# Kernel optimization log

Hardware: AMD Instinct MI355X
Metric: run time of the kernel (lower is better)

Reference implementation:

```python
import jax, jax.numpy as jnp
import numpy as np

C = 64          # num_channels
DEPTH = 9       # dilation_depth
REPEAT = 2      # dilation_repeat
K = 2           # kernel_size
DILATIONS = [2 ** j for _ in range(REPEAT) for j in range(DEPTH)]
L = len(DILATIONS)  # 18 gated layers


def causal_conv(x, w, b, dilation):
    # x: [B, Cin, T], w: [Cout, Cin, K] -> [B, Cout, T] with causal (left) padding
    pad = (w.shape[-1] - 1) * dilation
    y = jax.lax.conv_general_dilated(
        x, w, window_strides=(1,), padding=[(pad, 0)],
        rhs_dilation=(dilation,), dimension_numbers=("NCH", "OIH", "NCH"))
    return y + b[None, :, None]


def setup_inputs() -> dict:
    key = jax.random.key(0)
    ks = jax.random.split(key, 9)
    s = 0.1
    x = jax.random.normal(ks[0], (4, 1, 65536), dtype=jnp.float32)
    in_w = jax.random.normal(ks[1], (C, 1, 1), dtype=jnp.float32) * s
    in_b = jax.random.normal(ks[2], (C,), dtype=jnp.float32) * s
    hid_w = jax.random.normal(ks[3], (L, 2 * C, C, K), dtype=jnp.float32) * s
    hid_b = jax.random.normal(ks[4], (L, 2 * C), dtype=jnp.float32) * s
    res_w = jax.random.normal(ks[5], (L, C, C, 1), dtype=jnp.float32) * s
    res_b = jax.random.normal(ks[6], (L, C), dtype=jnp.float32) * s
    mix_w = jax.random.normal(ks[7], (1, C * L, 1), dtype=jnp.float32) * s
    mix_b = jax.random.normal(ks[8], (1,), dtype=jnp.float32) * s
    return {"x": x, "in_w": in_w, "in_b": in_b, "hid_w": hid_w, "hid_b": hid_b,
            "res_w": res_w, "res_b": res_b, "mix_w": mix_w, "mix_b": mix_b}


def reference(x, in_w, in_b, hid_w, hid_b, res_w, res_b, mix_w, mix_b):
    # Input 1x1 conv: [B,1,T] -> [B,C,T]
    out = causal_conv(x, in_w, in_b, 1)
    skips = []
    for i, d in enumerate(DILATIONS):
        xi = out
        h = causal_conv(xi, hid_w[i], hid_b[i], d)       # [B, 2C, T]
        gated = jnp.tanh(h[:, :C]) * jax.nn.sigmoid(h[:, C:])  # [B, C, T]
        skips.append(gated)
        out = causal_conv(gated, res_w[i], res_b[i], 1) + xi    # residual
    skip = jnp.concatenate(skips, axis=1)                # [B, C*L, T]
    return causal_conv(skip, mix_w, mix_b, 1)            # [B, 1, T]
```

## Files before the change

### kernel.cpp

```cpp
#include <hip/hip_runtime.h>
#include <hip/hip_bf16.h>
#include <math.h>

#define NCH 64
#define T_LEN 65536
#define NLAYER 18

typedef __attribute__((ext_vector_type(8))) short bf16x8;
typedef __attribute__((ext_vector_type(4))) short bf16x4;
typedef __attribute__((ext_vector_type(4))) float f32x4;

static __device__ __forceinline__ float bf2f(short s) {
    union { short u[2]; float f; } v;
    v.u[0] = 0; v.u[1] = s;
    return v.f;
}
static __device__ __forceinline__ short f2bf(float f) {
    __hip_bfloat16 h = __float2bfloat16(f);
    return *(short*)&h;
}

__global__ void convert_weights_kernel(const float* __restrict__ hid_w,
                                       const float* __restrict__ res_w,
                                       __hip_bfloat16* __restrict__ whid,
                                       __hip_bfloat16* __restrict__ wres) {
    int gid = blockIdx.x * 256 + threadIdx.x;
    if (gid < NLAYER * 128 * 128) {
        int l   = gid >> 14;
        int rem = gid & 16383;
        int o   = rem >> 7;
        int k   = rem & 127;
        float v = (k < 64)
            ? hid_w[((l * 128 + o) * 64 + k) * 2]
            : hid_w[((l * 128 + o) * 64 + (k - 64)) * 2 + 1];
        whid[gid] = __float2bfloat16(v);
    }
    if (gid < NLAYER * 64 * 64) {
        wres[gid] = __float2bfloat16(res_w[gid]);
    }
}

__global__ __launch_bounds__(256, 2) void fused6_kernel(
    const void* __restrict__ src,
    __hip_bfloat16* __restrict__ next,
    float* __restrict__ acc,
    const __hip_bfloat16* __restrict__ whid_all,
    const float* __restrict__ hb_all,
    const __hip_bfloat16* __restrict__ wres_all,
    const float* __restrict__ rb_all,
    const float* __restrict__ mix_w,
    const float* __restrict__ in_w,
    const float* __restrict__ in_b,
    int lbase, int is_first) {
    __shared__ __align__(16) __hip_bfloat16 A[192 * 72];
    __shared__ __align__(16) __hip_bfloat16 G[192 * 72];

    const int b    = blockIdx.x >> 9;
    const int widx = blockIdx.x & 511;
    const int t0   = widx << 7;
    const int tw   = t0 - 64;

    const int tid  = threadIdx.x;
    const int lane = tid & 63;
    const int w4   = tid >> 6;
    const int l15  = lane & 15;
    const int quad = lane >> 4;
    const int m0   = w4 * 16;
    const int rr   = tid >> 3;
    const int co   = (tid & 7) * 8;

    if (is_first) {
        const float* x = (const float*)src;
        float iw[8], ib[8];
#pragma unroll
        for (int j = 0; j < 8; ++j) { iw[j] = in_w[co + j]; ib[j] = in_b[co + j]; }
#pragma unroll
        for (int round = 0; round < 6; ++round) {
            int r  = round * 32 + rr;
            int gt = tw + r;
            bf16x8 v = {0, 0, 0, 0, 0, 0, 0, 0};
            if (gt >= 0) {
                float xv = x[(size_t)b * T_LEN + gt];
#pragma unroll
                for (int j = 0; j < 8; ++j) v[j] = f2bf(iw[j] * xv + ib[j]);
            }
            *(bf16x8*)(&A[r * 72 + co]) = v;
        }
    } else {
        const __hip_bfloat16* prev = (const __hip_bfloat16*)src;
#pragma unroll
        for (int round = 0; round < 6; ++round) {
            int r  = round * 32 + rr;
            int gt = tw + r;
            bf16x8 v = {0, 0, 0, 0, 0, 0, 0, 0};
            if (gt >= 0)
                v = *(const bf16x8*)(prev + ((size_t)b * T_LEN + gt) * NCH + co);
            *(bf16x8*)(&A[r * 72 + co]) = v;
        }
    }

    float skacc0 = 0.f, skacc1 = 0.f;

#pragma unroll 1
    for (int l = 0; l < 6; ++l) {
        const int d = 1 << l;
        const __hip_bfloat16* whid = whid_all + (size_t)(lbase + l) * 16384;
        const __hip_bfloat16* wres = wres_all + (size_t)(lbase + l) * 4096;
        const float* hb = hb_all + (lbase + l) * 128;
        const float* rb = rb_all + (lbase + l) * 64;
        const float* mw = mix_w + (lbase + l) * 64;

        bf16x8 aT[4], aS[4], aR[2];
        {
            const __hip_bfloat16* whT = whid + (size_t)(m0 + l15) * 128 + quad * 8;
            const __hip_bfloat16* whS = whT + 64 * 128;
#pragma unroll
            for (int k = 0; k < 4; ++k) {
                aT[k] = *(const bf16x8*)(whT + k * 32);
                aS[k] = *(const bf16x8*)(whS + k * 32);
            }
            const __hip_bfloat16* wrA = wres + (size_t)(m0 + l15) * 64 + quad * 8;
            aR[0] = *(const bf16x8*)(wrA);
            aR[1] = *(const bf16x8*)(wrA + 32);
        }
        f32x4 biasT, biasS, biasR;
#pragma unroll
        for (int r = 0; r < 4; ++r) {
            biasT[r] = hb[m0 + quad * 4 + r];
            biasS[r] = hb[64 + m0 + quad * 4 + r];
            biasR[r] = rb[m0 + quad * 4 + r];
        }
        float mwq[16];
#pragma unroll
        for (int k = 0; k < 4; ++k) {
            float4 m4 = *(const float4*)(mw + quad * 16 + k * 4);
            mwq[k * 4 + 0] = m4.x; mwq[k * 4 + 1] = m4.y;
            mwq[k * 4 + 2] = m4.z; mwq[k * 4 + 3] = m4.w;
        }

        __syncthreads();

#pragma unroll
        for (int ct = 0; ct < 3; ++ct) {
            f32x4 accT[4], accS[4];
#pragma unroll
            for (int nt = 0; nt < 4; ++nt) { accT[nt] = biasT; accS[nt] = biasS; }
#pragma unroll
            for (int ks = 0; ks < 4; ++ks) {
                const int koff = (ks & 1) * 32 + quad * 8;
#pragma unroll
                for (int nt = 0; nt < 4; ++nt) {
                    int trow = ct * 64 + nt * 16 + l15;
                    int prow = trow - d;  prow = prow < 0 ? 0 : prow;
                    int row  = (ks < 2) ? prow : trow;
                    bf16x8 bx = *(const bf16x8*)(&A[row * 72 + koff]);
                    accT[nt] = __builtin_amdgcn_mfma_f32_16x16x32_bf16(aT[ks], bx, accT[nt], 0, 0, 0);
                    accS[nt] = __builtin_amdgcn_mfma_f32_16x16x32_bf16(aS[ks], bx, accS[nt], 0, 0, 0);
                }
            }
#pragma unroll
            for (int nt = 0; nt < 4; ++nt) {
                int trow = ct * 64 + nt * 16 + l15;
                bf16x4 gv;
#pragma unroll
                for (int r = 0; r < 4; ++r) {
                    float e2 = __expf(2.f * accT[nt][r]);
                    float th = 1.f - 2.f * __builtin_amdgcn_rcpf(e2 + 1.f);
                    float sg = __builtin_amdgcn_rcpf(1.f + __expf(-accS[nt][r]));
                    gv[r] = f2bf(th * sg);
                }
                *(bf16x4*)(&G[trow * 72 + m0 + quad * 4]) = gv;
            }
        }
        __syncthreads();

#pragma unroll
        for (int ct = 0; ct < 3; ++ct) {
            f32x4 accR[4];
#pragma unroll
            for (int nt = 0; nt < 4; ++nt) accR[nt] = biasR;
#pragma unroll
            for (int ks = 0; ks < 2; ++ks) {
                const int koff = ks * 32 + quad * 8;
#pragma unroll
                for (int nt = 0; nt < 4; ++nt) {
                    int trow = ct * 64 + nt * 16 + l15;
                    bf16x8 bx = *(const bf16x8*)(&G[trow * 72 + koff]);
                    accR[nt] = __builtin_amdgcn_mfma_f32_16x16x32_bf16(aR[ks], bx, accR[nt], 0, 0, 0);
                }
            }
#pragma unroll
            for (int nt = 0; nt < 4; ++nt) {
                int trow = ct * 64 + nt * 16 + l15;
                bf16x4 old = *(const bf16x4*)(&A[trow * 72 + m0 + quad * 4]);
                bool ok = (tw + trow) >= 0;
                bf16x4 ov;
#pragma unroll
                for (int r = 0; r < 4; ++r) {
                    float v = accR[nt][r] + bf2f(old[r]);
                    ov[r] = f2bf(ok ? v : 0.f);
                }
                *(bf16x4*)(&A[trow * 72 + m0 + quad * 4]) = ov;
            }
        }

#pragma unroll
        for (int s = 0; s < 2; ++s) {
            int p = 64 + w4 * 32 + s * 16 + l15;
            bf16x8 g0 = *(const bf16x8*)(&G[p * 72 + quad * 16]);
            bf16x8 g1 = *(const bf16x8*)(&G[p * 72 + quad * 16 + 8]);
            float sv = 0.f;
#pragma unroll
            for (int j = 0; j < 8; ++j) {
                sv += mwq[j]     * bf2f(g0[j]);
                sv += mwq[8 + j] * bf2f(g1[j]);
            }
            if (s == 0) skacc0 += sv; else skacc1 += sv;
        }
    }
    __syncthreads();

#pragma unroll
    for (int round = 0; round < 4; ++round) {
        int pr = round * 32 + rr;
        *(bf16x8*)(next + ((size_t)b * T_LEN + t0 + pr) * NCH + co) =
            *(const bf16x8*)(&A[(pr + 64) * 72 + co]);
    }

    skacc0 += __shfl_xor(skacc0, 16, 64);
    skacc0 += __shfl_xor(skacc0, 32, 64);
    skacc1 += __shfl_xor(skacc1, 16, 64);
    skacc1 += __shfl_xor(skacc1, 32, 64);
    if (quad == 0) {
        acc[(size_t)b * T_LEN + t0 + w4 * 32 + l15]      += skacc0;
        acc[(size_t)b * T_LEN + t0 + w4 * 32 + 16 + l15] += skacc1;
    }
}

__global__ __launch_bounds__(256, 2) void layer_mfma_kernel(
    const __hip_bfloat16* __restrict__ prev,
    __hip_bfloat16* __restrict__ next,
    float* __restrict__ acc,
    const __hip_bfloat16* __restrict__ whid,
    const float* __restrict__ hb,
    const __hip_bfloat16* __restrict__ wres,
    const float* __restrict__ rb,
    const float* __restrict__ mw,
    int d) {
    __shared__ __align__(16) __hip_bfloat16 Xp[64 * 72];
    __shared__ __align__(16) __hip_bfloat16 Xc[64 * 72];
    __shared__ __align__(16) __hip_bfloat16 Gt[64 * 72];

    const int t0   = blockIdx.x << 6;
    const int tid  = threadIdx.x;
    const int lane = tid & 63;
    const int w4   = tid >> 6;
    const int l15  = lane & 15;
    const int quad = lane >> 4;
    const int m0   = w4 * 16;
    const int rr = tid >> 3;
    const int co = (tid & 7) * 8;

    bf16x8 aT[4], aS[4], aR[2];
    {
        const __hip_bfloat16* whT = whid + (size_t)(m0 + l15) * 128 + quad * 8;
        const __hip_bfloat16* whS = whT + 64 * 128;
#pragma unroll
        for (int k = 0; k < 4; ++k) {
            aT[k] = *(const bf16x8*)(whT + k * 32);
            aS[k] = *(const bf16x8*)(whS + k * 32);
        }
        const __hip_bfloat16* wrA = wres + (size_t)(m0 + l15) * 64 + quad * 8;
        aR[0] = *(const bf16x8*)(wrA);
        aR[1] = *(const bf16x8*)(wrA + 32);
    }
    f32x4 biasT, biasS, biasR;
#pragma unroll
    for (int r = 0; r < 4; ++r) {
        biasT[r] = hb[m0 + quad * 4 + r];
        biasS[r] = hb[64 + m0 + quad * 4 + r];
        biasR[r] = rb[m0 + quad * 4 + r];
    }
    float mwq[16];
#pragma unroll
    for (int j = 0; j < 16; ++j) mwq[j] = mw[quad * 16 + j];

    bf16x8 pc[2], pp[2];
#define LOAD_TILE(b)                                                          \
    do {                                                                      \
        const __hip_bfloat16* pb = prev + ((size_t)(b) * T_LEN + t0) * NCH;   \
        _Pragma("unroll")                                                     \
        for (int pass = 0; pass < 2; ++pass) {                                \
            int r = pass * 32 + rr;                                           \
            pc[pass] = *(const bf16x8*)(pb + r * NCH + co);                   \
            int tp = t0 + r - d;                                              \
            bf16x8 z = {0, 0, 0, 0, 0, 0, 0, 0};                              \
            pp[pass] = z;                                                     \
            if (tp >= 0)                                                      \
                pp[pass] = *(const bf16x8*)(prev +                            \
                    ((size_t)(b) * T_LEN + tp) * NCH + co);                   \
        }                                                                     \
    } while (0)

    LOAD_TILE(0);

#pragma unroll
    for (int b = 0; b < 4; ++b) {
#pragma unroll
        for (int pass = 0; pass < 2; ++pass) {
            int r = pass * 32 + rr;
            *(bf16x8*)(&Xc[r * 72 + co]) = pc[pass];
            *(bf16x8*)(&Xp[r * 72 + co]) = pp[pass];
        }
        __syncthreads();

        if (b < 3) LOAD_TILE(b + 1);

        f32x4 accT[4], accS[4];
#pragma unroll
        for (int nt = 0; nt < 4; ++nt) { accT[nt] = biasT; accS[nt] = biasS; }
#pragma unroll
        for (int ks = 0; ks < 4; ++ks) {
            const __hip_bfloat16* srcb = (ks < 2) ? Xp : Xc;
            const int kk = (ks & 1) * 32 + quad * 8;
#pragma unroll
            for (int nt = 0; nt < 4; ++nt) {
                bf16x8 bx = *(const bf16x8*)(&srcb[(nt * 16 + l15) * 72 + kk]);
                accT[nt] = __builtin_amdgcn_mfma_f32_16x16x32_bf16(aT[ks], bx, accT[nt], 0, 0, 0);
                accS[nt] = __builtin_amdgcn_mfma_f32_16x16x32_bf16(aS[ks], bx, accS[nt], 0, 0, 0);
            }
        }

#pragma unroll
        for (int nt = 0; nt < 4; ++nt) {
            int t = nt * 16 + l15;
#pragma unroll
            for (int r = 0; r < 4; ++r) {
                float e2 = __expf(2.f * accT[nt][r]);
                float th = 1.f - 2.f * __builtin_amdgcn_rcpf(e2 + 1.f);
                float sg = __builtin_amdgcn_rcpf(1.f + __expf(-accS[nt][r]));
                Gt[t * 72 + m0 + quad * 4 + r] = __float2bfloat16(th * sg);
            }
        }

        bf16x4 curres[4];
#pragma unroll
        for (int nt = 0; nt < 4; ++nt) {
            curres[nt] = *(const bf16x4*)(&Xc[(nt * 16 + l15) * 72 + m0 + quad * 4]);
        }
        __syncthreads();

        f32x4 accR[4];
#pragma unroll
        for (int nt = 0; nt < 4; ++nt) accR[nt] = biasR;
#pragma unroll
        for (int ks = 0; ks < 2; ++ks) {
            const int kk = ks * 32 + quad * 8;
#pragma unroll
            for (int nt = 0; nt < 4; ++nt) {
                bf16x8 bx = *(const bf16x8*)(&Gt[(nt * 16 + l15) * 72 + kk]);
                accR[nt] = __builtin_amdgcn_mfma_f32_16x16x32_bf16(aR[ks], bx, accR[nt], 0, 0, 0);
            }
        }

        __hip_bfloat16* nb = next + ((size_t)b * T_LEN + t0) * NCH;
#pragma unroll
        for (int nt = 0; nt < 4; ++nt) {
            int t = nt * 16 + l15;
            bf16x4 ov;
#pragma unroll
            for (int r = 0; r < 4; ++r) {
                ov[r] = f2bf(accR[nt][r] + bf2f(curres[nt][r]));
            }
            *(bf16x4*)(nb + t * NCH + m0 + quad * 4) = ov;
        }

        {
            int t = w4 * 16 + l15;
            bf16x8 g0 = *(const bf16x8*)(&Gt[t * 72 + quad * 16]);
            bf16x8 g1 = *(const bf16x8*)(&Gt[t * 72 + quad * 16 + 8]);
            float s = 0.f;
#pragma unroll
            for (int j = 0; j < 8; ++j) {
                s += mwq[j]     * bf2f(g0[j]);
                s += mwq[8 + j] * bf2f(g1[j]);
            }
            s += __shfl_xor(s, 16, 64);
            s += __shfl_xor(s, 32, 64);
            if (quad == 0)
                acc[(size_t)b * T_LEN + t0 + t] += s;
        }
    }
#undef LOAD_TILE
}

__global__ __launch_bounds__(256, 2) void last_layer_kernel(
    const __hip_bfloat16* __restrict__ prev,
    const float* __restrict__ acc,
    float* __restrict__ out,
    const __hip_bfloat16* __restrict__ whid,
    const float* __restrict__ hb,
    const float* __restrict__ mw,
    const float* __restrict__ mix_b,
    int d) {
    __shared__ __align__(16) __hip_bfloat16 Xp[64 * 72];
    __shared__ __align__(16) __hip_bfloat16 Xc[64 * 72];
    __shared__ float skb[4 * 64];

    const int t0   = blockIdx.x << 6;
    const int tid  = threadIdx.x;
    const int lane = tid & 63;
    const int w4   = tid >> 6;
    const int l15  = lane & 15;
    const int quad = lane >> 4;
    const int m0   = w4 * 16;
    const int rr = tid >> 3;
    const int co = (tid & 7) * 8;

    bf16x8 aT[4], aS[4];
    {
        const __hip_bfloat16* whT = whid + (size_t)(m0 + l15) * 128 + quad * 8;
        const __hip_bfloat16* whS = whT + 64 * 128;
#pragma unroll
        for (int k = 0; k < 4; ++k) {
            aT[k] = *(const bf16x8*)(whT + k * 32);
            aS[k] = *(const bf16x8*)(whS + k * 32);
        }
    }
    f32x4 biasT, biasS;
    float mwv[4];
#pragma unroll
    for (int r = 0; r < 4; ++r) {
        biasT[r] = hb[m0 + quad * 4 + r];
        biasS[r] = hb[64 + m0 + quad * 4 + r];
        mwv[r]   = mw[m0 + quad * 4 + r];
    }
    const float mb = mix_b[0];

    bf16x8 pc[2], pp[2];
#define LOAD_TILE(b)                                                          \
    do {                                                                      \
        const __hip_bfloat16* pb = prev + ((size_t)(b) * T_LEN + t0) * NCH;   \
        _Pragma("unroll")                                                     \
        for (int pass = 0; pass < 2; ++pass) {                                \
            int r = pass * 32 + rr;                                           \
            pc[pass] = *(const bf16x8*)(pb + r * NCH + co);                   \
            int tp = t0 + r - d;                                              \
            bf16x8 z = {0, 0, 0, 0, 0, 0, 0, 0};                              \
            pp[pass] = z;                                                     \
            if (tp >= 0)                                                      \
                pp[pass] = *(const bf16x8*)(prev +                            \
                    ((size_t)(b) * T_LEN + tp) * NCH + co);                   \
        }                                                                     \
    } while (0)

    LOAD_TILE(0);

#pragma unroll
    for (int b = 0; b < 4; ++b) {
#pragma unroll
        for (int pass = 0; pass < 2; ++pass) {
            int r = pass * 32 + rr;
            *(bf16x8*)(&Xc[r * 72 + co]) = pc[pass];
            *(bf16x8*)(&Xp[r * 72 + co]) = pp[pass];
        }
        __syncthreads();

        if (b < 3) LOAD_TILE(b + 1);

        f32x4 accT[4], accS[4];
#pragma unroll
        for (int nt = 0; nt < 4; ++nt) { accT[nt] = biasT; accS[nt] = biasS; }
#pragma unroll
        for (int ks = 0; ks < 4; ++ks) {
            const __hip_bfloat16* srcb = (ks < 2) ? Xp : Xc;
            const int kk = (ks & 1) * 32 + quad * 8;
#pragma unroll
            for (int nt = 0; nt < 4; ++nt) {
                bf16x8 bx = *(const bf16x8*)(&srcb[(nt * 16 + l15) * 72 + kk]);
                accT[nt] = __builtin_amdgcn_mfma_f32_16x16x32_bf16(aT[ks], bx, accT[nt], 0, 0, 0);
                accS[nt] = __builtin_amdgcn_mfma_f32_16x16x32_bf16(aS[ks], bx, accS[nt], 0, 0, 0);
            }
        }

#pragma unroll
        for (int nt = 0; nt < 4; ++nt) {
            float sv = 0.f;
#pragma unroll
            for (int r = 0; r < 4; ++r) {
                float e2 = __expf(2.f * accT[nt][r]);
                float th = 1.f - 2.f * __builtin_amdgcn_rcpf(e2 + 1.f);
                float sg = __builtin_amdgcn_rcpf(1.f + __expf(-accS[nt][r]));
                sv += mwv[r] * (th * sg);
            }
            sv += __shfl_xor(sv, 16, 64);
            sv += __shfl_xor(sv, 32, 64);
            if (quad == 0)
                skb[w4 * 64 + nt * 16 + l15] = sv;
        }
        __syncthreads();

        if (tid < 64) {
            float tot = skb[tid] + skb[64 + tid] + skb[128 + tid] + skb[192 + tid];
            out[(size_t)b * T_LEN + t0 + tid] =
                acc[(size_t)b * T_LEN + t0 + tid] + tot + mb;
        }
    }
#undef LOAD_TILE
}

extern "C" void kernel_launch(void* const* d_in, const int* in_sizes, int n_in,
                              void* d_out, int out_size, void* d_ws, size_t ws_size,
                              hipStream_t stream) {
    const float* x     = (const float*)d_in[0];
    const float* in_w  = (const float*)d_in[1];
    const float* in_b  = (const float*)d_in[2];
    const float* hid_w = (const float*)d_in[3];
    const float* hid_b = (const float*)d_in[4];
    const float* res_w = (const float*)d_in[5];
    const float* res_b = (const float*)d_in[6];
    const float* mix_w = (const float*)d_in[7];
    const float* mix_b = (const float*)d_in[8];
    float* out = (float*)d_out;

    const size_t act_elems = 4ull * T_LEN * NCH;
    __hip_bfloat16* actA = (__hip_bfloat16*)d_ws;
    __hip_bfloat16* actB = actA + act_elems;
    float* acc = (float*)(actB + act_elems);
    __hip_bfloat16* whid = (__hip_bfloat16*)(acc + 4ull * T_LEN);
    __hip_bfloat16* wres = whid + (size_t)NLAYER * 128 * 128;

    hipMemsetAsync(acc, 0, 4ull * T_LEN * sizeof(float), stream);

    convert_weights_kernel<<<1152, 256, 0, stream>>>(hid_w, res_w, whid, wres);

    fused6_kernel<<<2048, 256, 0, stream>>>(
        x, actA, acc, whid, hid_b, wres, res_b, mix_w, in_w, in_b, 0, 1);

    layer_mfma_kernel<<<1024, 256, 0, stream>>>(
        actA, actB, acc, whid + 6 * 16384, hid_b + 6 * 128,
        wres + 6 * 4096, res_b + 6 * 64, mix_w + 6 * 64, 64);
    layer_mfma_kernel<<<1024, 256, 0, stream>>>(
        actB, actA, acc, whid + 7 * 16384, hid_b + 7 * 128,
        wres + 7 * 4096, res_b + 7 * 64, mix_w + 7 * 64, 128);
    layer_mfma_kernel<<<1024, 256, 0, stream>>>(
        actA, actB, acc, whid + 8 * 16384, hid_b + 8 * 128,
        wres + 8 * 4096, res_b + 8 * 64, mix_w + 8 * 64, 256);

    fused6_kernel<<<2048, 256, 0, stream>>>(
        actB, actA, acc, whid, hid_b, wres, res_b, mix_w, in_w, in_b, 9, 0);

    layer_mfma_kernel<<<1024, 256, 0, stream>>>(
        actA, actB, acc, whid + 15 * 16384, hid_b + 15 * 128,
        wres + 15 * 4096, res_b + 15 * 64, mix_w + 15 * 64, 64);
    layer_mfma_kernel<<<1024, 256, 0, stream>>>(
        actB, actA, acc, whid + 16 * 16384, hid_b + 16 * 128,
        wres + 16 * 4096, res_b + 16 * 64, mix_w + 16 * 64, 128);

    last_layer_kernel<<<1024, 256, 0, stream>>>(
        actA, acc, out, whid + 17 * 16384, hid_b + 17 * 128,
        mix_w + 17 * 64, mix_b, 256);
}
```

Baseline: 559.0 us.

## Swizzle LDS tiles, fuse skip mix into gate epilogue, raise occupancy

Replaces the padded 72-stride LDS layout with a 64-stride XOR-swizzled layout, which shrinks shared memory enough to allow three blocks per CU and is meant to avoid bank conflicts. The skip-mix dot product is computed directly from the fp32 gate values in the gate epilogue, so the separate LDS re-read of G is gone; partial sums are reduced across waves through LDS at the end. The gate math is merged into one reciprocal per element. The skip now uses unrounded fp32 values rather than bf16, and the higher launch bound may cause register spills.

```diff
diff --git a/kernel.cpp b/kernel.cpp
--- a/kernel.cpp
+++ b/kernel.cpp
@@ -40,7 +40,7 @@
     }
 }
 
-__global__ __launch_bounds__(256, 2) void fused6_kernel(
+__global__ __launch_bounds__(256, 3) void fused6_kernel(
     const void* __restrict__ src,
     __hip_bfloat16* __restrict__ next,
     float* __restrict__ acc,
@@ -52,8 +52,10 @@
     const float* __restrict__ in_w,
     const float* __restrict__ in_b,
     int lbase, int is_first) {
-    __shared__ __align__(16) __hip_bfloat16 A[192 * 72];
-    __shared__ __align__(16) __hip_bfloat16 G[192 * 72];
+    __shared__ __align__(16) __hip_bfloat16 A[192 * 64];
+    __shared__ __align__(16) __hip_bfloat16 G[192 * 64];
+
+#define SW(row, col) ((row) * 64 + ((col) ^ (((row) & 7) << 3)))
 
     const int b    = blockIdx.x >> 9;
     const int widx = blockIdx.x & 511;
@@ -84,7 +86,7 @@
 #pragma unroll
                 for (int j = 0; j < 8; ++j) v[j] = f2bf(iw[j] * xv + ib[j]);
             }
-            *(bf16x8*)(&A[r * 72 + co]) = v;
+            *(bf16x8*)(&A[SW(r, co)]) = v;
         }
     } else {
         const __hip_bfloat16* prev = (const __hip_bfloat16*)src;
@@ -95,11 +97,11 @@
             bf16x8 v = {0, 0, 0, 0, 0, 0, 0, 0};
             if (gt >= 0)
                 v = *(const bf16x8*)(prev + ((size_t)b * T_LEN + gt) * NCH + co);
-            *(bf16x8*)(&A[r * 72 + co]) = v;
-        }
-    }
-
-    float skacc0 = 0.f, skacc1 = 0.f;
+            *(bf16x8*)(&A[SW(r, co)]) = v;
+        }
+    }
+
+    float skp[8] = {0.f, 0.f, 0.f, 0.f, 0.f, 0.f, 0.f, 0.f};
 
 #pragma unroll 1
     for (int l = 0; l < 6; ++l) {
@@ -130,13 +132,7 @@
             biasS[r] = hb[64 + m0 + quad * 4 + r];
             biasR[r] = rb[m0 + quad * 4 + r];
         }
-        float mwq[16];
-#pragma unroll
-        for (int k = 0; k < 4; ++k) {
-            float4 m4 = *(const float4*)(mw + quad * 16 + k * 4);
-            mwq[k * 4 + 0] = m4.x; mwq[k * 4 + 1] = m4.y;
-            mwq[k * 4 + 2] = m4.z; mwq[k * 4 + 3] = m4.w;
-        }
+        f32x4 mw4 = *(const f32x4*)(mw + m0 + quad * 4);
 
         __syncthreads();
 
@@ -153,7 +149,7 @@
                     int trow = ct * 64 + nt * 16 + l15;
                     int prow = trow - d;  prow = prow < 0 ? 0 : prow;
                     int row  = (ks < 2) ? prow : trow;
-                    bf16x8 bx = *(const bf16x8*)(&A[row * 72 + koff]);
+                    bf16x8 bx = *(const bf16x8*)(&A[SW(row, koff)]);
                     accT[nt] = __builtin_amdgcn_mfma_f32_16x16x32_bf16(aT[ks], bx, accT[nt], 0, 0, 0);
                     accS[nt] = __builtin_amdgcn_mfma_f32_16x16x32_bf16(aS[ks], bx, accS[nt], 0, 0, 0);
                 }
@@ -162,14 +158,18 @@
             for (int nt = 0; nt < 4; ++nt) {
                 int trow = ct * 64 + nt * 16 + l15;
                 bf16x4 gv;
+                float gsum = 0.f;
 #pragma unroll
                 for (int r = 0; r < 4; ++r) {
-                    float e2 = __expf(2.f * accT[nt][r]);
-                    float th = 1.f - 2.f * __builtin_amdgcn_rcpf(e2 + 1.f);
-                    float sg = __builtin_amdgcn_rcpf(1.f + __expf(-accS[nt][r]));
-                    gv[r] = f2bf(th * sg);
+                    float ea = __expf(2.f * accT[nt][r]);
+                    float eb = __expf(-accS[nt][r]);
+                    float g  = (ea - 1.f) *
+                               __builtin_amdgcn_rcpf((ea + 1.f) * (1.f + eb));
+                    gsum += mw4[r] * g;
+                    gv[r] = f2bf(g);
                 }
-                *(bf16x4*)(&G[trow * 72 + m0 + quad * 4]) = gv;
+                if (ct >= 1) skp[(ct - 1) * 4 + nt] += gsum;
+                *(bf16x4*)(&G[SW(trow, m0 + quad * 4)]) = gv;
             }
         }
         __syncthreads();
@@ -185,14 +185,14 @@
 #pragma unroll
                 for (int nt = 0; nt < 4; ++nt) {
                     int trow = ct * 64 + nt * 16 + l15;
-                    bf16x8 bx = *(const bf16x8*)(&G[trow * 72 + koff]);
+                    bf16x8 bx = *(const bf16x8*)(&G[SW(trow, koff)]);
                     accR[nt] = __builtin_amdgcn_mfma_f32_16x16x32_bf16(aR[ks], bx, accR[nt], 0, 0, 0);
                 }
             }
 #pragma unroll
             for (int nt = 0; nt < 4; ++nt) {
                 int trow = ct * 64 + nt * 16 + l15;
-                bf16x4 old = *(const bf16x4*)(&A[trow * 72 + m0 + quad * 4]);
+                bf16x4 old = *(const bf16x4*)(&A[SW(trow, m0 + quad * 4)]);
                 bool ok = (tw + trow) >= 0;
                 bf16x4 ov;
 #pragma unroll
@@ -200,22 +200,8 @@
                     float v = accR[nt][r] + bf2f(old[r]);
                     ov[r] = f2bf(ok ? v : 0.f);
                 }
-                *(bf16x4*)(&A[trow * 72 + m0 + quad * 4]) = ov;
-            }
-        }
-
-#pragma unroll
-        for (int s = 0; s < 2; ++s) {
-            int p = 64 + w4 * 32 + s * 16 + l15;
-            bf16x8 g0 = *(const bf16x8*)(&G[p * 72 + quad * 16]);
-            bf16x8 g1 = *(const bf16x8*)(&G[p * 72 + quad * 16 + 8]);
-            float sv = 0.f;
-#pragma unroll
-            for (int j = 0; j < 8; ++j) {
-                sv += mwq[j]     * bf2f(g0[j]);
-                sv += mwq[8 + j] * bf2f(g1[j]);
-            }
-            if (s == 0) skacc0 += sv; else skacc1 += sv;
+                *(bf16x4*)(&A[SW(trow, m0 + quad * 4)]) = ov;
+            }
         }
     }
     __syncthreads();
@@ -224,17 +210,29 @@
     for (int round = 0; round < 4; ++round) {
         int pr = round * 32 + rr;
         *(bf16x8*)(next + ((size_t)b * T_LEN + t0 + pr) * NCH + co) =
-            *(const bf16x8*)(&A[(pr + 64) * 72 + co]);
-    }
-
-    skacc0 += __shfl_xor(skacc0, 16, 64);
-    skacc0 += __shfl_xor(skacc0, 32, 64);
-    skacc1 += __shfl_xor(skacc1, 16, 64);
-    skacc1 += __shfl_xor(skacc1, 32, 64);
+            *(const bf16x8*)(&A[SW(pr + 64, co)]);
+    }
+
+    float* skbuf = (float*)G;
+#pragma unroll
+    for (int i = 0; i < 8; ++i) {
+        skp[i] += __shfl_xor(skp[i], 16, 64);
+        skp[i] += __shfl_xor(skp[i], 32, 64);
+    }
     if (quad == 0) {
-        acc[(size_t)b * T_LEN + t0 + w4 * 32 + l15]      += skacc0;
-        acc[(size_t)b * T_LEN + t0 + w4 * 32 + 16 + l15] += skacc1;
-    }
+#pragma unroll
+        for (int i = 0; i < 8; ++i) {
+            int ct = i >> 2, nt = i & 3;
+            skbuf[w4 * 128 + ct * 64 + nt * 16 + l15] = skp[i];
+        }
+    }
+    __syncthreads();
+    if (tid < 128) {
+        float tot = skbuf[tid] + skbuf[128 + tid] +
+                    skbuf[256 + tid] + skbuf[384 + tid];
+        acc[(size_t)b * T_LEN + t0 + tid] += tot;
+    }
+#undef SW
 }
 
 __global__ __launch_bounds__(256, 2) void layer_mfma_kernel(
```

After: 530.4 us. -5.1%, faster.
